# Kernel tuning notes

Hardware: AMD Instinct MI355X
Metric: run time of the kernel (lower is better)

## Reference

```python
import jax, jax.numpy as jnp
import numpy as np

N = 100000
E = 1600000
D_IN = 50
D_H = 128
D_OUT = 128
EPS = 1e-5


def setup_inputs() -> dict:
    key = jax.random.key(0)
    ks = jax.random.split(key, 24)
    def w(k, shape, fan_in):
        return jax.random.normal(k, shape, jnp.float32) / np.sqrt(fan_in)
    inp = {
        'x': jax.random.normal(ks[0], (N, D_IN), jnp.float32),
        'edge_src': jax.random.randint(ks[1], (E,), 0, N, jnp.int32),
        'edge_dst': jax.random.randint(ks[2], (E,), 0, N, jnp.int32),
        # SAGEConv 1: D_IN -> D_H
        'Wl1': w(ks[3], (D_IN, D_H), D_IN), 'Wr1': w(ks[4], (D_IN, D_H), D_IN), 'b1': jnp.zeros((D_H,), jnp.float32),
        # SAGEConv 2: D_H -> D_H
        'Wl2': w(ks[5], (D_H, D_H), D_H), 'Wr2': w(ks[6], (D_H, D_H), D_H), 'b2': jnp.zeros((D_H,), jnp.float32),
        # SAGEConv 3: D_H -> D_OUT
        'Wl3': w(ks[7], (D_H, D_OUT), D_H), 'Wr3': w(ks[8], (D_H, D_OUT), D_H), 'b3': jnp.zeros((D_OUT,), jnp.float32),
        # skip linears (no bias)
        'Ws1': w(ks[9], (D_IN, D_H), D_IN), 'Ws2': w(ks[10], (D_IN, D_H), D_IN),
        # LayerNorm affine
        'lnw1': jnp.ones((D_H,), jnp.float32), 'lnb1': jnp.zeros((D_H,), jnp.float32),
        'lnw2': jnp.ones((D_H,), jnp.float32), 'lnb2': jnp.zeros((D_H,), jnp.float32),
        'lnw3': jnp.ones((D_OUT,), jnp.float32), 'lnb3': jnp.zeros((D_OUT,), jnp.float32),
        # PReLU scalar slopes (PyG init 0.25)
        'a1': jnp.float32(0.25), 'a2': jnp.float32(0.25), 'a3': jnp.float32(0.25),
    }
    return inp


def _sage(x, src, dst, Wl, Wr, b):
    # mean aggregation of source features at destinations, then linear + root
    msg = x[src]                                              # [E, d]
    agg = jax.ops.segment_sum(msg, dst, num_segments=N)       # [N, d]
    cnt = jax.ops.segment_sum(jnp.ones((src.shape[0],), x.dtype), dst, num_segments=N)
    mean = agg / jnp.maximum(cnt, 1.0)[:, None]
    return mean @ Wl + x @ Wr + b


def _graph_ln(x, w, b):
    # PyG LayerNorm mode='graph', batch=None: normalize over all nodes+channels
    xc = x - jnp.mean(x)
    std = jnp.sqrt(jnp.mean(xc * xc))
    return (xc / (std + EPS)) * w + b


def _prelu(x, a):
    return jnp.where(x >= 0, x, a * x)


def reference(x, edge_src, edge_dst, Wl1, Wr1, b1, Wl2, Wr2, b2, Wl3, Wr3, b3,
              Ws1, Ws2, lnw1, lnb1, lnw2, lnb2, lnw3, lnb3, a1, a2, a3):
    h1 = _sage(x, edge_src, edge_dst, Wl1, Wr1, b1)
    h1 = _prelu(_graph_ln(h1, lnw1, lnb1), a1)
    h2 = _sage(h1 + x @ Ws1, edge_src, edge_dst, Wl2, Wr2, b2)
    h2 = _prelu(_graph_ln(h2, lnw2, lnb2), a2)
    ret = _sage(h1 + h2 + x @ Ws2, edge_src, edge_dst, Wl3, Wr3, b3)
    ret = _prelu(_graph_ln(ret, lnw3, lnb3), a3)
    return ret
```

## Files before the change

kernel.cpp:

```cpp
#include <hip/hip_runtime.h>

#define D_IN 50
#define LN_EPS 1e-5f
#define BSH 8
#define MAXB 512

typedef __bf16 bf16_t;
typedef bf16_t bf16x8 __attribute__((ext_vector_type(8)));
typedef bf16_t bf16x4 __attribute__((ext_vector_type(4)));
typedef bf16_t bf16x2 __attribute__((ext_vector_type(2)));
typedef float f32x4_t __attribute__((ext_vector_type(4)));
typedef float f32x2_t __attribute__((ext_vector_type(2)));

#define ACCP(r, A)                                                            \
    {                                                                         \
        A[0] += (f32x2_t){__uint_as_float((r).x << 16),                       \
                          __uint_as_float((r).x & 0xffff0000u)};              \
        A[1] += (f32x2_t){__uint_as_float((r).y << 16),                       \
                          __uint_as_float((r).y & 0xffff0000u)};              \
        A[2] += (f32x2_t){__uint_as_float((r).z << 16),                       \
                          __uint_as_float((r).z & 0xffff0000u)};              \
        A[3] += (f32x2_t){__uint_as_float((r).w << 16),                       \
                          __uint_as_float((r).w & 0xffff0000u)};              \
    }

__global__ void bucket_hist_k(const int* __restrict__ dst, int* __restrict__ bcnt,
                              int e, int nb) {
    __shared__ int lh[MAXB];
    int t = threadIdx.x;
    for (int i = t; i < nb; i += 256) lh[i] = 0;
    __syncthreads();
    for (int i = blockIdx.x * 256 + t; i < e; i += gridDim.x * 256)
        atomicAdd(&lh[dst[i] >> BSH], 1);
    __syncthreads();
    for (int i = t; i < nb; i += 256) {
        int c = lh[i];
        if (c) atomicAdd(&bcnt[i * 16], c);
    }
}

__global__ void bscan_k(const int* __restrict__ bcnt, int* __restrict__ boff,
                        int* __restrict__ bpos, int nb, int e) {
    __shared__ int l[MAXB];
    int t = threadIdx.x;
    l[t] = (t < nb) ? bcnt[t * 16] : 0;
    __syncthreads();
    for (int off = 1; off < MAXB; off <<= 1) {
        int v = (t >= off) ? l[t - off] : 0;
        __syncthreads();
        l[t] += v;
        __syncthreads();
    }
    int excl = (t > 0) ? l[t - 1] : 0;
    if (t < nb) { boff[t] = excl; bpos[t * 16] = excl; }
    if (t == 0) boff[nb] = e;
}

__global__ void scatter_k(const int* __restrict__ src, const int* __restrict__ dst,
                          int* __restrict__ bpos, unsigned* __restrict__ pool,
                          int e, int nb) {
    __shared__ int lh[MAXB];
    __shared__ int lcur[MAXB];
    int t = threadIdx.x;
    for (int i = t; i < nb; i += 256) lh[i] = 0;
    __syncthreads();
    int chunk = (e + gridDim.x - 1) / gridDim.x;
    int s = blockIdx.x * chunk;
    int en = min(e, s + chunk);
    for (int i = s + t; i < en; i += 256)
        atomicAdd(&lh[dst[i] >> BSH], 1);
    __syncthreads();
    for (int i = t; i < nb; i += 256) {
        int c = lh[i];
        lcur[i] = c ? atomicAdd(&bpos[i * 16], c) : 0;
    }
    __syncthreads();
    for (int i = s + t; i < en; i += 256) {
        int d = dst[i];
        int p = atomicAdd(&lcur[d >> BSH], 1);
        pool[p] = (unsigned)src[i] | ((unsigned)(d & 255) << 17);
    }
}

__global__ void nhist_rp_k(const unsigned* __restrict__ pool, const int* __restrict__ boff,
                           int* __restrict__ rp, int n) {
    __shared__ int lc[256];
    __shared__ int ls[256];
    int b = blockIdx.x, t = threadIdx.x;
    lc[t] = 0;
    __syncthreads();
    int s = boff[b], e = boff[b + 1];
    for (int i = s + t; i < e; i += 256) atomicAdd(&lc[pool[i] >> 17], 1);
    __syncthreads();
    int v = lc[t];
    ls[t] = v;
    __syncthreads();
    for (int off = 1; off < 256; off <<= 1) {
        int x = (t >= off) ? ls[t - off] : 0;
        __syncthreads();
        ls[t] += x;
        __syncthreads();
    }
    int excl = ls[t] - v;
    int nd = (b << BSH) + t;
    if (nd < n) rp[nd] = s + excl;
    if (nd == n - 1) rp[n] = e;
}

__global__ void cfill_k(const unsigned* __restrict__ pool, const int* __restrict__ boff,
                        const int* __restrict__ rp, int* __restrict__ col, int n) {
    __shared__ int lpos[256];
    int b = blockIdx.x, t = threadIdx.x;
    int nd = (b << BSH) + t;
    lpos[t] = (nd < n) ? rp[nd] : 0;
    __syncthreads();
    int s = boff[b], e = boff[b + 1];
    for (int i = s + t; i < e; i += 256) {
        unsigned pk = pool[i];
        int slot = atomicAdd(&lpos[pk >> 17], 1);
        col[slot] = (int)(pk & 0x1FFFFu);
    }
}

struct ConvDesc { const float* w; bf16_t* o; int kin; int kpad; };
struct ConvArgs { ConvDesc d[8]; };

__global__ void conv_w_k(ConvArgs args) {
    ConvDesc d = args.d[blockIdx.y];
    int i = blockIdx.x * 256 + threadIdx.x;
    int tot = 128 * d.kpad;
    if (i >= tot) return;
    int n = i / d.kpad, k = i - n * d.kpad;
    float v = (k < d.kin) ? d.w[(size_t)k * 128 + n] : 0.f;
    d.o[i] = (bf16_t)v;
}

__global__ void conv_x_k(const float* __restrict__ x, bf16_t* __restrict__ xb, int n) {
    int i = blockIdx.x * 256 + threadIdx.x;
    if (i >= n * 64) return;
    int node = i >> 6, k = i & 63;
    xb[i] = (k < D_IN) ? (bf16_t)x[node * D_IN + k] : (bf16_t)0.f;
}

__global__ void agg_bf64_k(const bf16_t* __restrict__ feat, const int* __restrict__ rp,
                           const int* __restrict__ col, bf16_t* __restrict__ mean, int n) {
    int wid = (blockIdx.x * blockDim.x + threadIdx.x) >> 6;
    int lane = threadIdx.x & 63;
    if (wid >= n) return;
    int start = rp[wid], end = rp[wid + 1];
    int lc = lane & 7;
    int g = lane >> 3;
    f32x2_t accA[4], accB[4];
#pragma unroll
    for (int k = 0; k < 4; k++) { accA[k] = (f32x2_t){0.f, 0.f}; accB[k] = (f32x2_t){0.f, 0.f}; }
    int e = start + g;
    if (e + 8 < end) {
        int i0 = col[e], i1 = col[e + 8];
        for (; e + 24 < end; e += 16) {
            uint4 r0 = *(const uint4*)(feat + (size_t)i0 * 64 + lc * 8);
            uint4 r1 = *(const uint4*)(feat + (size_t)i1 * 64 + lc * 8);
            i0 = col[e + 16];
            i1 = col[e + 24];
            ACCP(r0, accA);
            ACCP(r1, accB);
        }
        uint4 r0 = *(const uint4*)(feat + (size_t)i0 * 64 + lc * 8);
        uint4 r1 = *(const uint4*)(feat + (size_t)i1 * 64 + lc * 8);
        ACCP(r0, accA);
        ACCP(r1, accB);
        e += 16;
    }
    for (; e < end; e += 8) {
        uint4 r0 = *(const uint4*)(feat + (size_t)col[e] * 64 + lc * 8);
        ACCP(r0, accA);
    }
#pragma unroll
    for (int k = 0; k < 4; k++) accA[k] += accB[k];
    float aL[4], aH[4];
#pragma unroll
    for (int k = 0; k < 4; k++) { aL[k] = accA[k].x; aH[k] = accA[k].y; }
#pragma unroll
    for (int off = 8; off < 64; off <<= 1) {
#pragma unroll
        for (int k = 0; k < 4; k++) {
            aL[k] += __shfl_xor(aL[k], off);
            aH[k] += __shfl_xor(aH[k], off);
        }
    }
    int c = end - start;
    float invc = 1.f / (float)(c > 0 ? c : 1);
    if (lane < 8) {
        bf16x8 o;
#pragma unroll
        for (int k = 0; k < 4; k++) {
            o[2 * k] = (bf16_t)(aL[k] * invc);
            o[2 * k + 1] = (bf16_t)(aH[k] * invc);
        }
        *(bf16x8*)(mean + (size_t)wid * 64 + lc * 8) = o;
    }
}

__global__ void agg_bf128_k(const bf16_t* __restrict__ feat, const int* __restrict__ rp,
                            const int* __restrict__ col, bf16_t* __restrict__ mean, int n) {
    int wid = (blockIdx.x * blockDim.x + threadIdx.x) >> 6;
    int lane = threadIdx.x & 63;
    if (wid >= n) return;
    int start = rp[wid], end = rp[wid + 1];
    int lc = lane & 15;
    int g = lane >> 4;
    f32x2_t accA[4], accB[4];
#pragma unroll
    for (int k = 0; k < 4; k++) { accA[k] = (f32x2_t){0.f, 0.f}; accB[k] = (f32x2_t){0.f, 0.f}; }
    int e = start + g;
    if (e + 4 < end) {
        int i0 = col[e], i1 = col[e + 4];
        for (; e + 12 < end; e += 8) {
            uint4 r0 = *(const uint4*)(feat + (size_t)i0 * 128 + lc * 8);
            uint4 r1 = *(const uint4*)(feat + (size_t)i1 * 128 + lc * 8);
            i0 = col[e + 8];
            i1 = col[e + 12];
            ACCP(r0, accA);
            ACCP(r1, accB);
        }
        uint4 r0 = *(const uint4*)(feat + (size_t)i0 * 128 + lc * 8);
        uint4 r1 = *(const uint4*)(feat + (size_t)i1 * 128 + lc * 8);
        ACCP(r0, accA);
        ACCP(r1, accB);
        e += 8;
    }
    for (; e < end; e += 4) {
        uint4 r0 = *(const uint4*)(feat + (size_t)col[e] * 128 + lc * 8);
        ACCP(r0, accA);
    }
#pragma unroll
    for (int k = 0; k < 4; k++) accA[k] += accB[k];
    float aL[4], aH[4];
#pragma unroll
    for (int k = 0; k < 4; k++) { aL[k] = accA[k].x; aH[k] = accA[k].y; }
#pragma unroll
    for (int off = 16; off < 64; off <<= 1) {
#pragma unroll
        for (int k = 0; k < 4; k++) {
            aL[k] += __shfl_xor(aL[k], off);
            aH[k] += __shfl_xor(aH[k], off);
        }
    }
    int c = end - start;
    float invc = 1.f / (float)(c > 0 ? c : 1);
    if (lane < 16) {
        bf16x8 o;
#pragma unroll
        for (int k = 0; k < 4; k++) {
            o[2 * k] = (bf16_t)(aL[k] * invc);
            o[2 * k + 1] = (bf16_t)(aH[k] * invc);
        }
        *(bf16x8*)(mean + (size_t)wid * 128 + lc * 8) = o;
    }
}

template <int KPAD, bool DUAL, bool ACC>
__global__ __launch_bounds__(256) void mfma_gemm_k(
    const bf16_t* __restrict__ A, const bf16_t* __restrict__ B,
    const bf16_t* __restrict__ WlT, const bf16_t* __restrict__ WrT,
    const float* __restrict__ bias,
    bf16_t* __restrict__ out, float2* __restrict__ partials, int M) {
    constexpr int KC = KPAD / 32;
    constexpr int WELE = 8 * KC * 64 * 8;
    __shared__ bf16_t lwl[WELE];
    __shared__ bf16_t lwr[DUAL ? WELE : 8];

    const int tid = threadIdx.x;
    for (int ch = tid; ch < 8 * KC * 64; ch += 256) {
        int nt = ch / (KC * 64);
        int rem = ch - nt * (KC * 64);
        int c = rem >> 6;
        int ln = rem & 63;
        int m = ln & 15, q = ln >> 4;
        size_t srcoff = (size_t)(nt * 16 + m) * KPAD + c * 32 + q * 8;
        *(bf16x8*)&lwl[ch * 8] = *(const bf16x8*)(WlT + srcoff);
        if (DUAL) *(bf16x8*)&lwr[ch * 8] = *(const bf16x8*)(WrT + srcoff);
    }
    __syncthreads();

    const int wid = blockIdx.x * 4 + (tid >> 6);
    const int lane = tid & 63;
    const int row0 = wid * 32;
    if (row0 >= M) return;
    const int m = lane & 15;
    const int q = lane >> 4;

    bf16x8 af[2][KC], bfr[DUAL ? 2 : 1][DUAL ? KC : 1];
#pragma unroll
    for (int s = 0; s < 2; s++) {
        const bf16_t* ar = A + (size_t)(row0 + s * 16 + m) * KPAD + q * 8;
#pragma unroll
        for (int c = 0; c < KC; c++) af[s][c] = *(const bf16x8*)(ar + c * 32);
        if (DUAL) {
            const bf16_t* br = B + (size_t)(row0 + s * 16 + m) * KPAD + q * 8;
#pragma unroll
            for (int c = 0; c < KC; c++) bfr[s][c] = *(const bf16x8*)(br + c * 32);
        }
    }

    float lsum = 0.f, lsum2 = 0.f;
#pragma unroll
    for (int nt = 0; nt < 8; nt++) {
        f32x4_t acc0 = {0.f, 0.f, 0.f, 0.f};
        f32x4_t acc1 = {0.f, 0.f, 0.f, 0.f};
#pragma unroll
        for (int c = 0; c < KC; c++) {
            bf16x8 w = *(const bf16x8*)&lwl[((nt * KC + c) * 64 + lane) * 8];
            acc0 = __builtin_amdgcn_mfma_f32_16x16x32_bf16(af[0][c], w, acc0, 0, 0, 0);
            acc1 = __builtin_amdgcn_mfma_f32_16x16x32_bf16(af[1][c], w, acc1, 0, 0, 0);
        }
        if (DUAL) {
#pragma unroll
            for (int c = 0; c < KC; c++) {
                bf16x8 w = *(const bf16x8*)&lwr[((nt * KC + c) * 64 + lane) * 8];
                acc0 = __builtin_amdgcn_mfma_f32_16x16x32_bf16(bfr[0][c], w, acc0, 0, 0, 0);
                acc1 = __builtin_amdgcn_mfma_f32_16x16x32_bf16(bfr[1][c], w, acc1, 0, 0, 0);
            }
        }
        float bv = bias ? bias[nt * 16 + m] : 0.f;
#pragma unroll
        for (int s = 0; s < 2; s++) {
            f32x4_t* ap = (s == 0) ? &acc0 : &acc1;
#pragma unroll
            for (int r = 0; r < 4; r++) {
                int row = row0 + s * 16 + q * 4 + r;
                if (row < M) {
                    float o = (*ap)[r] + bv;
                    out[(size_t)row * 128 + nt * 16 + m] = (bf16_t)o;
                    if (ACC) { lsum += o; lsum2 += o * o; }
                }
            }
        }
    }
    if (ACC) {
        for (int off = 32; off > 0; off >>= 1) {
            lsum += __shfl_down(lsum, off);
            lsum2 += __shfl_down(lsum2, off);
        }
        if (lane == 0) partials[wid] = make_float2(lsum, lsum2);
    }
}

__global__ __launch_bounds__(256) void mfma_gemm3_k(
    const bf16_t* __restrict__ A, const bf16_t* __restrict__ B,
    const bf16_t* __restrict__ WlT, const bf16_t* __restrict__ WrT,
    const bf16_t* __restrict__ Ws1T, const bf16_t* __restrict__ Ws2T,
    const float* __restrict__ bias,
    bf16_t* __restrict__ outP, bf16_t* __restrict__ outC1, bf16_t* __restrict__ outC2,
    float2* __restrict__ partials, int M) {
    constexpr int KC = 2;
    constexpr int WELE = 8 * KC * 64 * 8;
    __shared__ bf16_t lwl[WELE];
    __shared__ bf16_t lwr[WELE];
    __shared__ bf16_t ls1[WELE];
    __shared__ bf16_t ls2[WELE];

    const int tid = threadIdx.x;
    for (int ch = tid; ch < 8 * KC * 64; ch += 256) {
        int nt = ch / (KC * 64);
        int rem = ch - nt * (KC * 64);
        int c = rem >> 6;
        int ln = rem & 63;
        int m = ln & 15, q = ln >> 4;
        size_t srcoff = (size_t)(nt * 16 + m) * 64 + c * 32 + q * 8;
        *(bf16x8*)&lwl[ch * 8] = *(const bf16x8*)(WlT + srcoff);
        *(bf16x8*)&lwr[ch * 8] = *(const bf16x8*)(WrT + srcoff);
        *(bf16x8*)&ls1[ch * 8] = *(const bf16x8*)(Ws1T + srcoff);
        *(bf16x8*)&ls2[ch * 8] = *(const bf16x8*)(Ws2T + srcoff);
    }
    __syncthreads();

    const int wid = blockIdx.x * 4 + (tid >> 6);
    const int lane = tid & 63;
    const int row0 = wid * 32;
    if (row0 >= M) return;
    const int m = lane & 15;
    const int q = lane >> 4;

    bf16x8 af[2][KC], bfr[2][KC];
#pragma unroll
    for (int s = 0; s < 2; s++) {
        const bf16_t* ar = A + (size_t)(row0 + s * 16 + m) * 64 + q * 8;
        const bf16_t* br = B + (size_t)(row0 + s * 16 + m) * 64 + q * 8;
#pragma unroll
        for (int c = 0; c < KC; c++) {
            af[s][c] = *(const bf16x8*)(ar + c * 32);
            bfr[s][c] = *(const bf16x8*)(br + c * 32);
        }
    }

    float lsum = 0.f, lsum2 = 0.f;
#pragma unroll
    for (int nt = 0; nt < 8; nt++) {
        f32x4_t aP0 = {0.f, 0.f, 0.f, 0.f}, aP1 = {0.f, 0.f, 0.f, 0.f};
        f32x4_t a10 = {0.f, 0.f, 0.f, 0.f}, a11 = {0.f, 0.f, 0.f, 0.f};
        f32x4_t a20 = {0.f, 0.f, 0.f, 0.f}, a21 = {0.f, 0.f, 0.f, 0.f};
#pragma unroll
        for (int c = 0; c < KC; c++) {
            int wi = ((nt * KC + c) * 64 + lane) * 8;
            bf16x8 wl = *(const bf16x8*)&lwl[wi];
            bf16x8 wr = *(const bf16x8*)&lwr[wi];
            bf16x8 w1 = *(const bf16x8*)&ls1[wi];
            bf16x8 w2 = *(const bf16x8*)&ls2[wi];
            aP0 = __builtin_amdgcn_mfma_f32_16x16x32_bf16(af[0][c], wl, aP0, 0, 0, 0);
            aP1 = __builtin_amdgcn_mfma_f32_16x16x32_bf16(af[1][c], wl, aP1, 0, 0, 0);
            aP0 = __builtin_amdgcn_mfma_f32_16x16x32_bf16(bfr[0][c], wr, aP0, 0, 0, 0);
            aP1 = __builtin_amdgcn_mfma_f32_16x16x32_bf16(bfr[1][c], wr, aP1, 0, 0, 0);
            a10 = __builtin_amdgcn_mfma_f32_16x16x32_bf16(bfr[0][c], w1, a10, 0, 0, 0);
            a11 = __builtin_amdgcn_mfma_f32_16x16x32_bf16(bfr[1][c], w1, a11, 0, 0, 0);
            a20 = __builtin_amdgcn_mfma_f32_16x16x32_bf16(bfr[0][c], w2, a20, 0, 0, 0);
            a21 = __builtin_amdgcn_mfma_f32_16x16x32_bf16(bfr[1][c], w2, a21, 0, 0, 0);
        }
        float bv = bias[nt * 16 + m];
#pragma unroll
        for (int s = 0; s < 2; s++) {
            f32x4_t* pP = (s == 0) ? &aP0 : &aP1;
            f32x4_t* p1 = (s == 0) ? &a10 : &a11;
            f32x4_t* p2 = (s == 0) ? &a20 : &a21;
#pragma unroll
            for (int r = 0; r < 4; r++) {
                int row = row0 + s * 16 + q * 4 + r;
                if (row < M) {
                    float o = (*pP)[r] + bv;
                    size_t oi = (size_t)row * 128 + nt * 16 + m;
                    outP[oi] = (bf16_t)o;
                    outC1[oi] = (bf16_t)(*p1)[r];
                    outC2[oi] = (bf16_t)(*p2)[r];
                    lsum += o; lsum2 += o * o;
                }
            }
        }
    }
    for (int off = 32; off > 0; off >>= 1) {
        lsum += __shfl_down(lsum, off);
        lsum2 += __shfl_down(lsum2, off);
    }
    if (lane == 0) partials[wid] = make_float2(lsum, lsum2);
}

__global__ void reduce_partials_k(const float2* __restrict__ p, int n,
                                  double* __restrict__ outp) {
    __shared__ double s1[256], s2[256];
    int t = threadIdx.x;
    double a = 0.0, b = 0.0;
    for (int i = t; i < n; i += 256) { a += (double)p[i].x; b += (double)p[i].y; }
    s1[t] = a; s2[t] = b;
    __syncthreads();
    for (int off = 128; off > 0; off >>= 1) {
        if (t < off) { s1[t] += s1[t + off]; s2[t] += s2[t + off]; }
        __syncthreads();
    }
    if (t == 0) { outp[0] = s1[0]; outp[1] = s2[0]; }
}

template <int MODE>
__global__ void ln_prelu_k(const bf16_t* __restrict__ pre, const bf16_t* __restrict__ h1in,
                           const bf16_t* __restrict__ s,
                           const float* __restrict__ lnw, const float* __restrict__ lnb,
                           const float* __restrict__ a_ptr, const double* __restrict__ acc,
                           void* __restrict__ out0v, void* __restrict__ out1v, int total) {
    int i = blockIdx.x * blockDim.x + threadIdx.x;
    if (i * 4 >= total) return;
    double cinv = 1.0 / (double)total;
    double mm = acc[0] * cinv;
    double var = acc[1] * cinv - mm * mm;
    float stdv = (float)sqrt(var > 0.0 ? var : 0.0);
    float scale = 1.0f / (stdv + LN_EPS);
    float mf = (float)mm;
    float a = a_ptr[0];
    int c4 = i & 31;
    float4 w = ((const float4*)lnw)[c4];
    float4 b = ((const float4*)lnb)[c4];
    bf16x4 p4 = ((const bf16x4*)pre)[i];
    float4 h;
    h.x = ((float)p4.x - mf) * scale * w.x + b.x;
    h.y = ((float)p4.y - mf) * scale * w.y + b.y;
    h.z = ((float)p4.z - mf) * scale * w.z + b.z;
    h.w = ((float)p4.w - mf) * scale * w.w + b.w;
    h.x = h.x >= 0.f ? h.x : a * h.x;
    h.y = h.y >= 0.f ? h.y : a * h.y;
    h.z = h.z >= 0.f ? h.z : a * h.z;
    h.w = h.w >= 0.f ? h.w : a * h.w;
    if (MODE == 1) {
        bf16x4 hb;
        hb.x = (bf16_t)h.x; hb.y = (bf16_t)h.y; hb.z = (bf16_t)h.z; hb.w = (bf16_t)h.w;
        ((bf16x4*)out0v)[i] = hb;
        bf16x4 sv = ((const bf16x4*)s)[i];
        bf16x4 tb;
        tb.x = (bf16_t)(h.x + (float)sv.x); tb.y = (bf16_t)(h.y + (float)sv.y);
        tb.z = (bf16_t)(h.z + (float)sv.z); tb.w = (bf16_t)(h.w + (float)sv.w);
        ((bf16x4*)out1v)[i] = tb;
    } else if (MODE == 2) {
        bf16x4 hv = ((const bf16x4*)h1in)[i];
        bf16x4 sv = ((const bf16x4*)s)[i];
        bf16x4 tb;
        tb.x = (bf16_t)((float)hv.x + h.x + (float)sv.x);
        tb.y = (bf16_t)((float)hv.y + h.y + (float)sv.y);
        tb.z = (bf16_t)((float)hv.z + h.z + (float)sv.z);
        tb.w = (bf16_t)((float)hv.w + h.w + (float)sv.w);
        ((bf16x4*)out0v)[i] = tb;
    } else {
        ((float4*)out0v)[i] = h;
    }
}

extern "C" void kernel_launch(void* const* d_in, const int* in_sizes, int n_in,
                              void* d_out, int out_size, void* d_ws, size_t ws_size,
                              hipStream_t stream) {
    const float* x    = (const float*)d_in[0];
    const int*   esrc = (const int*)d_in[1];
    const int*   edst = (const int*)d_in[2];
    const float* Wl1  = (const float*)d_in[3];
    const float* Wr1  = (const float*)d_in[4];
    const float* b1   = (const float*)d_in[5];
    const float* Wl2  = (const float*)d_in[6];
    const float* Wr2  = (const float*)d_in[7];
    const float* b2   = (const float*)d_in[8];
    const float* Wl3  = (const float*)d_in[9];
    const float* Wr3  = (const float*)d_in[10];
    const float* b3   = (const float*)d_in[11];
    const float* Ws1  = (const float*)d_in[12];
    const float* Ws2  = (const float*)d_in[13];
    const float* lnw1 = (const float*)d_in[14];
    const float* lnb1 = (const float*)d_in[15];
    const float* lnw2 = (const float*)d_in[16];
    const float* lnb2 = (const float*)d_in[17];
    const float* lnw3 = (const float*)d_in[18];
    const float* lnb3 = (const float*)d_in[19];
    const float* a1   = (const float*)d_in[20];
    const float* a2   = (const float*)d_in[21];
    const float* a3   = (const float*)d_in[22];

    const int N = in_sizes[0] / D_IN;
    const int E = in_sizes[1];
    const int NB = (N + 255) >> BSH;

    char* ws = (char*)d_ws;
    size_t off = 0;
    auto alloc = [&](size_t bytes) -> void* {
        void* p = ws + off;
        off += (bytes + 255) & ~(size_t)255;
        return p;
    };
    bf16_t* xb   = (bf16_t*)alloc((size_t)N * 64 * 2);
    bf16_t* mean = (bf16_t*)alloc((size_t)N * 128 * 2);
    bf16_t* PRE  = (bf16_t*)alloc((size_t)N * 128 * 2);
    bf16_t* C1   = (bf16_t*)alloc((size_t)N * 128 * 2);
    bf16_t* C2   = (bf16_t*)alloc((size_t)N * 128 * 2);
    bf16_t* h1b  = (bf16_t*)alloc((size_t)N * 128 * 2);
    bf16_t* TB   = (bf16_t*)alloc((size_t)N * 128 * 2);
    bf16_t* WT   = (bf16_t*)alloc((size_t)(4 * 128 * 64 + 4 * 128 * 128) * 2);
    int* rp   = (int*)alloc((size_t)(N + 1) * 4);
    int* col  = (int*)alloc((size_t)E * 4);
    int* bcnt = (int*)alloc((size_t)MAXB * 16 * 4);
    int* boff = (int*)alloc((size_t)(MAXB + 1) * 4);
    int* bpos = (int*)alloc((size_t)MAXB * 16 * 4);
    unsigned* pool = (unsigned*)alloc((size_t)E * 4);
    double* lnacc = (double*)alloc(6 * 8);
    const int tiles = (N + 31) / 32;
    float2* partials = (float2*)alloc((size_t)tiles * 8);

    bf16_t* Wl1T = WT;
    bf16_t* Wr1T = Wl1T + 128 * 64;
    bf16_t* Ws1T = Wr1T + 128 * 64;
    bf16_t* Ws2T = Ws1T + 128 * 64;
    bf16_t* Wl2T = Ws2T + 128 * 64;
    bf16_t* Wr2T = Wl2T + 128 * 128;
    bf16_t* Wl3T = Wr2T + 128 * 128;
    bf16_t* Wr3T = Wl3T + 128 * 128;

    hipMemsetAsync(bcnt, 0, (size_t)MAXB * 16 * 4, stream);

    bucket_hist_k<<<256, 256, 0, stream>>>(edst, bcnt, E, NB);
    bscan_k<<<1, MAXB, 0, stream>>>(bcnt, boff, bpos, NB, E);
    scatter_k<<<256, 256, 0, stream>>>(esrc, edst, bpos, pool, E, NB);
    nhist_rp_k<<<NB, 256, 0, stream>>>(pool, boff, rp, N);
    cfill_k<<<NB, 256, 0, stream>>>(pool, boff, rp, col, N);

    ConvArgs ca;
    ca.d[0] = {Wl1, Wl1T, 50, 64};
    ca.d[1] = {Wr1, Wr1T, 50, 64};
    ca.d[2] = {Ws1, Ws1T, 50, 64};
    ca.d[3] = {Ws2, Ws2T, 50, 64};
    ca.d[4] = {Wl2, Wl2T, 128, 128};
    ca.d[5] = {Wr2, Wr2T, 128, 128};
    ca.d[6] = {Wl3, Wl3T, 128, 128};
    ca.d[7] = {Wr3, Wr3T, 128, 128};
    conv_w_k<<<dim3(64, 8), 256, 0, stream>>>(ca);
    conv_x_k<<<(N * 64 + 255) / 256, 256, 0, stream>>>(x, xb, N);

    const int aggBlocks = ((N * 64) + 255) / 256;
    const int gemmBlocks = (tiles + 3) / 4;
    const int lnBlocks = (N * 128 / 4 + 255) / 256;
    const int total = N * 128;

    agg_bf64_k<<<aggBlocks, 256, 0, stream>>>(xb, rp, col, mean, N);
    mfma_gemm3_k<<<gemmBlocks, 256, 0, stream>>>(
        mean, xb, Wl1T, Wr1T, Ws1T, Ws2T, b1, PRE, C1, C2, partials, N);
    reduce_partials_k<<<1, 256, 0, stream>>>(partials, tiles, lnacc + 0);
    ln_prelu_k<1><<<lnBlocks, 256, 0, stream>>>(
        PRE, nullptr, C1, lnw1, lnb1, a1, lnacc + 0, h1b, TB, total);

    agg_bf128_k<<<aggBlocks, 256, 0, stream>>>(TB, rp, col, mean, N);
    mfma_gemm_k<128, true, true><<<gemmBlocks, 256, 0, stream>>>(
        mean, TB, Wl2T, Wr2T, b2, PRE, partials, N);
    reduce_partials_k<<<1, 256, 0, stream>>>(partials, tiles, lnacc + 2);
    ln_prelu_k<2><<<lnBlocks, 256, 0, stream>>>(
        PRE, h1b, C2, lnw2, lnb2, a2, lnacc + 2, TB, nullptr, total);

    agg_bf128_k<<<aggBlocks, 256, 0, stream>>>(TB, rp, col, mean, N);
    mfma_gemm_k<128, true, true><<<gemmBlocks, 256, 0, stream>>>(
        mean, TB, Wl3T, Wr3T, b3, PRE, partials, N);
    reduce_partials_k<<<1, 256, 0, stream>>>(partials, tiles, lnacc + 4);
    ln_prelu_k<3><<<lnBlocks, 256, 0, stream>>>(
        PRE, nullptr, nullptr, lnw3, lnb3, a3, lnacc + 4, d_out, nullptr, total);
}
```

Baseline: 546.2 us.

## Fuse CSR histogram with column fill, unroll 128-wide gather, widen LN vectors

Merges the per-bucket node histogram/row-pointer kernel with the column-fill kernel so each block reuses its local prefix sums from shared memory, saving one launch and a re-read of the pool and rp. The 128-channel aggregation loop is restructured to issue four independent row loads per iteration, with a masked tail, to raise memory-level parallelism. The LayerNorm/PReLU kernel now processes 8 bf16 elements per thread with 16-byte accesses. Together these aim to reduce launch count and latency stalls in gather-heavy and elementwise stages, at the cost of more registers in the gather loop.

```diff
diff --git a/kernel.cpp b/kernel.cpp
--- a/kernel.cpp
+++ b/kernel.cpp
@@ -82,10 +82,11 @@
     }
 }
 
-__global__ void nhist_rp_k(const unsigned* __restrict__ pool, const int* __restrict__ boff,
-                           int* __restrict__ rp, int n) {
+__global__ void nhist_cfill_k(const unsigned* __restrict__ pool, const int* __restrict__ boff,
+                              int* __restrict__ rp, int* __restrict__ col, int n) {
     __shared__ int lc[256];
     __shared__ int ls[256];
+    __shared__ int lpos[256];
     int b = blockIdx.x, t = threadIdx.x;
     lc[t] = 0;
     __syncthreads();
@@ -105,16 +106,8 @@
     int nd = (b << BSH) + t;
     if (nd < n) rp[nd] = s + excl;
     if (nd == n - 1) rp[n] = e;
-}
-
-__global__ void cfill_k(const unsigned* __restrict__ pool, const int* __restrict__ boff,
-                        const int* __restrict__ rp, int* __restrict__ col, int n) {
-    __shared__ int lpos[256];
-    int b = blockIdx.x, t = threadIdx.x;
-    int nd = (b << BSH) + t;
-    lpos[t] = (nd < n) ? rp[nd] : 0;
-    __syncthreads();
-    int s = boff[b], e = boff[b + 1];
+    lpos[t] = s + excl;
+    __syncthreads();
     for (int i = s + t; i < e; i += 256) {
         unsigned pk = pool[i];
         int slot = atomicAdd(&lpos[pk >> 17], 1);
@@ -208,29 +201,35 @@
     int start = rp[wid], end = rp[wid + 1];
     int lc = lane & 15;
     int g = lane >> 4;
+    const uint* fp = (const uint*)feat + lc * 4;
     f32x2_t accA[4], accB[4];
 #pragma unroll
     for (int k = 0; k < 4; k++) { accA[k] = (f32x2_t){0.f, 0.f}; accB[k] = (f32x2_t){0.f, 0.f}; }
     int e = start + g;
-    if (e + 4 < end) {
-        int i0 = col[e], i1 = col[e + 4];
-        for (; e + 12 < end; e += 8) {
-            uint4 r0 = *(const uint4*)(feat + (size_t)i0 * 128 + lc * 8);
-            uint4 r1 = *(const uint4*)(feat + (size_t)i1 * 128 + lc * 8);
-            i0 = col[e + 8];
-            i1 = col[e + 12];
-            ACCP(r0, accA);
-            ACCP(r1, accB);
-        }
-        uint4 r0 = *(const uint4*)(feat + (size_t)i0 * 128 + lc * 8);
-        uint4 r1 = *(const uint4*)(feat + (size_t)i1 * 128 + lc * 8);
+    int ng = (e < end) ? (((end - 1 - e) >> 2) + 1) : 0;
+    int it = 0;
+    for (; it + 4 <= ng; it += 4, e += 16) {
+        int a = col[e], b = col[e + 4], c = col[e + 8], d = col[e + 12];
+        uint4 r0 = *(const uint4*)(fp + (size_t)a * 64);
+        uint4 r1 = *(const uint4*)(fp + (size_t)b * 64);
+        uint4 r2 = *(const uint4*)(fp + (size_t)c * 64);
+        uint4 r3 = *(const uint4*)(fp + (size_t)d * 64);
         ACCP(r0, accA);
         ACCP(r1, accB);
-        e += 8;
-    }
-    for (; e < end; e += 4) {
-        uint4 r0 = *(const uint4*)(feat + (size_t)col[e] * 128 + lc * 8);
+        ACCP(r2, accA);
+        ACCP(r3, accB);
+    }
+    int rem = ng - it;
+    if (rem > 0) {
+        int a = col[e];
+        int b = (rem > 1) ? col[e + 4] : a;
+        int c = (rem > 2) ? col[e + 8] : b;
+        uint4 r0 = *(const uint4*)(fp + (size_t)a * 64);
+        uint4 r1 = *(const uint4*)(fp + (size_t)b * 64);
+        uint4 r2 = *(const uint4*)(fp + (size_t)c * 64);
         ACCP(r0, accA);
+        if (rem > 1) ACCP(r1, accB);
+        if (rem > 2) ACCP(r2, accA);
     }
 #pragma unroll
     for (int k = 0; k < 4; k++) accA[k] += accB[k];
@@ -464,7 +463,7 @@
                            const float* __restrict__ a_ptr, const double* __restrict__ acc,
                            void* __restrict__ out0v, void* __restrict__ out1v, int total) {
     int i = blockIdx.x * blockDim.x + threadIdx.x;
-    if (i * 4 >= total) return;
+    if (i * 8 >= total) return;
     double cinv = 1.0 / (double)total;
     double mm = acc[0] * cinv;
     double var = acc[1] * cinv - mm * mm;
@@ -472,39 +471,43 @@
     float scale = 1.0f / (stdv + LN_EPS);
     float mf = (float)mm;
     float a = a_ptr[0];
-    int c4 = i & 31;
-    float4 w = ((const float4*)lnw)[c4];
-    float4 b = ((const float4*)lnb)[c4];
-    bf16x4 p4 = ((const bf16x4*)pre)[i];
-    float4 h;
-    h.x = ((float)p4.x - mf) * scale * w.x + b.x;
-    h.y = ((float)p4.y - mf) * scale * w.y + b.y;
-    h.z = ((float)p4.z - mf) * scale * w.z + b.z;
-    h.w = ((float)p4.w - mf) * scale * w.w + b.w;
-    h.x = h.x >= 0.f ? h.x : a * h.x;
-    h.y = h.y >= 0.f ? h.y : a * h.y;
-    h.z = h.z >= 0.f ? h.z : a * h.z;
-    h.w = h.w >= 0.f ? h.w : a * h.w;
+    int c8 = i & 15;
+    float4 w0 = ((const float4*)lnw)[c8 * 2];
+    float4 w1 = ((const float4*)lnw)[c8 * 2 + 1];
+    float4 b0 = ((const float4*)lnb)[c8 * 2];
+    float4 b1 = ((const float4*)lnb)[c8 * 2 + 1];
+    float wv[8] = {w0.x, w0.y, w0.z, w0.w, w1.x, w1.y, w1.z, w1.w};
+    float bv[8] = {b0.x, b0.y, b0.z, b0.w, b1.x, b1.y, b1.z, b1.w};
+    bf16x8 p8 = ((const bf16x8*)pre)[i];
+    float h[8];
+#pragma unroll
+    for (int k = 0; k < 8; k++) {
+        float v = ((float)p8[k] - mf) * scale * wv[k] + bv[k];
+        h[k] = v >= 0.f ? v : a * v;
+    }
     if (MODE == 1) {
-        bf16x4 hb;
-        hb.x = (bf16_t)h.x; hb.y = (bf16_t)h.y; hb.z = (bf16_t)h.z; hb.w = (bf16_t)h.w;
-        ((bf16x4*)out0v)[i] = hb;
-        bf16x4 sv = ((const bf16x4*)s)[i];
-        bf16x4 tb;
-        tb.x = (bf16_t)(h.x + (float)sv.x); tb.y = (bf16_t)(h.y + (float)sv.y);
-        tb.z = (bf16_t)(h.z + (float)sv.z); tb.w = (bf16_t)(h.w + (float)sv.w);
-        ((bf16x4*)out1v)[i] = tb;
+        bf16x8 hb, tb;
+        bf16x8 sv = ((const bf16x8*)s)[i];
+#pragma unroll
+        for (int k = 0; k < 8; k++) {
+            hb[k] = (bf16_t)h[k];
+            tb[k] = (bf16_t)(h[k] + (float)sv[k]);
+        }
+        ((bf16x8*)out0v)[i] = hb;
+        ((bf16x8*)out1v)[i] = tb;
     } else if (MODE == 2) {
-        bf16x4 hv = ((const bf16x4*)h1in)[i];
-        bf16x4 sv = ((const bf16x4*)s)[i];
-        bf16x4 tb;
-        tb.x = (bf16_t)((float)hv.x + h.x + (float)sv.x);
-        tb.y = (bf16_t)((float)hv.y + h.y + (float)sv.y);
-        tb.z = (bf16_t)((float)hv.z + h.z + (float)sv.z);
-        tb.w = (bf16_t)((float)hv.w + h.w + (float)sv.w);
-        ((bf16x4*)out0v)[i] = tb;
+        bf16x8 hv = ((const bf16x8*)h1in)[i];
+        bf16x8 sv = ((const bf16x8*)s)[i];
+        bf16x8 tb;
+#pragma unroll
+        for (int k = 0; k < 8; k++)
+            tb[k] = (bf16_t)((float)hv[k] + h[k] + (float)sv[k]);
+        ((bf16x8*)out0v)[i] = tb;
     } else {
-        ((float4*)out0v)[i] = h;
+        float4 o0 = {h[0], h[1], h[2], h[3]};
+        float4 o1 = {h[4], h[5], h[6], h[7]};
+        ((float4*)out0v)[i * 2] = o0;
+        ((float4*)out0v)[i * 2 + 1] = o1;
     }
 }
 
@@ -578,8 +581,7 @@
     bucket_hist_k<<<256, 256, 0, stream>>>(edst, bcnt, E, NB);
     bscan_k<<<1, MAXB, 0, stream>>>(bcnt, boff, bpos, NB, E);
     scatter_k<<<256, 256, 0, stream>>>(esrc, edst, bpos, pool, E, NB);
-    nhist_rp_k<<<NB, 256, 0, stream>>>(pool, boff, rp, N);
-    cfill_k<<<NB, 256, 0, stream>>>(pool, boff, rp, col, N);
+    nhist_cfill_k<<<NB, 256, 0, stream>>>(pool, boff, rp, col, N);
 
     ConvArgs ca;
     ca.d[0] = {Wl1, Wl1T, 50, 64};
@@ -595,7 +597,7 @@
 
     const int aggBlocks = ((N * 64) + 255) / 256;
     const int gemmBlocks = (tiles + 3) / 4;
-    const int lnBlocks = (N * 128 / 4 + 255) / 256;
+    const int lnBlocks = (N * 128 / 8 + 255) / 256;
     const int total = N * 128;
 
     agg_bf64_k<<<aggBlocks, 256, 0, stream>>>(xb, rp, col, mean, N);
```

Measured after the change: 538.1 us. No clear change (-1.5%).
